# Kernel tuning notes

Hardware: AMD Instinct MI355X
Metric: run time of the kernel (lower is better)

Reference implementation:

```python
import jax, jax.numpy as jnp
import numpy as np

N_NODES = 50000
N_EDGES = 800000


def setup_inputs() -> dict:
    key = jax.random.key(0)
    ks = jax.random.split(key, 12)
    x = jax.random.normal(ks[0], (N_NODES, 500), dtype=jnp.float32)
    edge_src = jax.random.randint(ks[1], (N_EDGES,), 0, N_NODES, dtype=jnp.int32)
    edge_dst = jax.random.randint(ks[2], (N_EDGES,), 0, N_NODES, dtype=jnp.int32)
    edge_vals = jax.random.uniform(ks[3], (N_EDGES,), dtype=jnp.float32) * 0.1
    def w(k, fan_in, fan_out):
        s = 1.0 / np.sqrt(fan_in)
        return jax.random.uniform(k, (fan_in, fan_out), dtype=jnp.float32, minval=-s, maxval=s)
    W1 = w(ks[4], 500, 128)
    b1 = jnp.zeros((128,), jnp.float32)
    W2 = w(ks[5], 128, 64)
    b2 = jnp.zeros((64,), jnp.float32)
    W3 = w(ks[6], 64, 16)
    b3 = jnp.zeros((16,), jnp.float32)
    We = w(ks[7], 64, 64)
    be = jnp.zeros((64,), jnp.float32)
    return {"x": x, "edge_vals": edge_vals, "W1": W1, "b1": b1, "W2": W2,
            "b2": b2, "W3": W3, "b3": b3, "We": We, "be": be,
            "edge_src": edge_src, "edge_dst": edge_dst}


def reference(x, edge_vals, W1, b1, W2, b2, W3, b3, We, be, edge_src, edge_dst):
    n = x.shape[0]

    def gcn_layer(h, W, b):
        # GraphConvolution: support = h @ W ; out = spmm(adj, support) + b
        support = h @ W                                   # [N, d_out]
        msg = support[edge_dst] * edge_vals[:, None]      # [E, d_out]
        agg = jax.ops.segment_sum(msg, edge_src, num_segments=n)
        return agg + b

    h = jax.nn.relu(gcn_layer(x, W1, b1))
    # dropout omitted (eval mode, training=False)
    h = jax.nn.relu(gcn_layer(h, W2, b2))
    out1 = jax.nn.log_softmax(gcn_layer(h, W3, b3), axis=1)
    out2 = h @ We + be
    return (out1, out2)
```

## Files before the change

kernel.cpp:

```cpp
#include <hip/hip_runtime.h>
#include <hip/hip_bf16.h>
#include <math.h>

#define N_NODES 50000
#define N_EDGES 800000

typedef __attribute__((ext_vector_type(8))) short bf16x8;
typedef __attribute__((ext_vector_type(4))) float f32x4;

__device__ inline unsigned short f2bf(float f) {
    unsigned u = __float_as_uint(f);
    unsigned r = (u + 0x7fffu + ((u >> 16) & 1u)) >> 16;
    return (unsigned short)r;
}

__device__ inline bf16x8 pack8(float4 a0, float4 a1) {
    union { __hip_bfloat162 h2[4]; bf16x8 v; } u;
    u.h2[0] = __float22bfloat162_rn(make_float2(a0.x, a0.y));
    u.h2[1] = __float22bfloat162_rn(make_float2(a0.z, a0.w));
    u.h2[2] = __float22bfloat162_rn(make_float2(a1.x, a1.y));
    u.h2[3] = __float22bfloat162_rn(make_float2(a1.z, a1.w));
    return u.v;
}

__global__ __launch_bounds__(256) void convert_hist_kernel(
    const float* __restrict__ W1, const float* __restrict__ W2,
    const float* __restrict__ We, const float* __restrict__ W3,
    unsigned short* __restrict__ W1frag, unsigned short* __restrict__ W2frag,
    unsigned short* __restrict__ Wcfrag,
    const int* __restrict__ src, int* __restrict__ counts)
{
    if (blockIdx.x < 308) {
        int t = blockIdx.x * 256 + threadIdx.x;
        if (t < 65536) {
            int h = t >> 15;
            int r1 = t & 32767;
            int j = r1 >> 13;
            int r2 = r1 & 8191;
            int s = r2 >> 9;
            int r3 = r2 & 511;
            int lane = r3 >> 3, jj = r3 & 7;
            int k = s * 32 + (lane >> 4) * 8 + jj;
            int n = h * 64 + j * 16 + (lane & 15);
            float v = (k < 500) ? W1[k * 128 + n] : 0.0f;
            W1frag[t] = f2bf(v);
        } else if (t < 73728) {
            int t2 = t - 65536;
            int j = t2 >> 11;
            int s = (t2 >> 9) & 3;
            int lane = (t2 >> 3) & 63, jj = t2 & 7;
            int k = s * 32 + (lane >> 4) * 8 + jj;
            int n = j * 16 + (lane & 15);
            W2frag[t2] = f2bf(W2[k * 64 + n]);
        } else {
            int t3 = t - 73728;
            int j = t3 >> 10;
            int s = (t3 >> 9) & 1;
            int lane = (t3 >> 3) & 63, jj = t3 & 7;
            int k = s * 32 + (lane >> 4) * 8 + jj;
            int n = j * 16 + (lane & 15);
            float v = (n < 64) ? We[k * 64 + n] : W3[k * 16 + (n - 64)];
            Wcfrag[t3] = f2bf(v);
        }
    } else {
        int e = (blockIdx.x - 308) * 256 + threadIdx.x;
        if (e < N_EDGES) atomicAdd(&counts[src[e]], 1);
    }
}

__global__ __launch_bounds__(1024) void scan_kernel(
    const int* __restrict__ counts, int* __restrict__ row_ptr,
    int* __restrict__ cursor)
{
    constexpr int Q = N_NODES / 4;
    const int t = threadIdx.x;
    const int lane = t & 63, wave = t >> 6;
    __shared__ int wsum[16];
    __shared__ int carry_s;
    int carry = 0;
    const int4* c4 = reinterpret_cast<const int4*>(counts);
    int4* rp4 = reinterpret_cast<int4*>(row_ptr);
    int4* cu4 = reinterpret_cast<int4*>(cursor);

    for (int base = 0; base < Q; base += 1024) {
        const int g = base + t;
        int4 v = {0, 0, 0, 0};
        if (g < Q) v = c4[g];
        const int s = v.x + v.y + v.z + v.w;

        int incl = s;
#pragma unroll
        for (int off = 1; off < 64; off <<= 1) {
            int n = __shfl_up(incl, off, 64);
            if (lane >= off) incl += n;
        }
        if (lane == 63) wsum[wave] = incl;
        __syncthreads();
        if (t < 16) {
            int w = wsum[t];
            int inc = w;
#pragma unroll
            for (int off = 1; off < 16; off <<= 1) {
                int n = __shfl_up(inc, off, 64);
                if (t >= off) inc += n;
            }
            wsum[t] = inc - w;
            if (t == 15) carry_s = inc;
        }
        __syncthreads();
        if (g < Q) {
            int e0 = carry + wsum[wave] + (incl - s);
            int4 r;
            r.x = e0;
            r.y = r.x + v.x;
            r.z = r.y + v.y;
            r.w = r.z + v.z;
            rp4[g] = r;
            cu4[g] = r;
        }
        carry += carry_s;
        __syncthreads();
    }
    if (t == 0) row_ptr[N_NODES] = carry;
}

__global__ __launch_bounds__(256) void fill_kernel(
    const int* __restrict__ src, const int* __restrict__ dst,
    const float* __restrict__ vals, int* __restrict__ cursor,
    int2* __restrict__ pairs)
{
    int e = blockIdx.x * 256 + threadIdx.x;
    if (e >= N_EDGES) return;
    int pos = atomicAdd(&cursor[src[e]], 1);
    pairs[pos] = make_int2(dst[e], __float_as_int(vals[e]));
}

__global__ __launch_bounds__(256, 2) void gemm1_mfma_kernel(
    const float* __restrict__ A,
    const unsigned short* __restrict__ W1frag,
    unsigned short* __restrict__ C)
{
    __shared__ __align__(16) unsigned short Bs[32768];

    const int t = threadIdx.x;
    const int h  = blockIdx.x & 1;
    const int br = blockIdx.x >> 1;
    const int lane = t & 63;
    const int wave = t >> 6;
    const int r = lane & 15, q = lane >> 4;

    {
        const uint4* src = reinterpret_cast<const uint4*>(W1frag + h * 32768);
        uint4* dst = reinterpret_cast<uint4*>(Bs);
#pragma unroll
        for (int i = 0; i < 16; ++i)
            dst[t + i * 256] = src[t + i * 256];
    }
    __syncthreads();

    const int col0 = h * 64;

    for (int c = br * 4 + wave; c < 3125; c += 1024) {
        const float* ap = A + (size_t)(c * 16 + r) * 500;

        f32x4 acc[4];
#pragma unroll
        for (int j = 0; j < 4; ++j) acc[j] = {0.f, 0.f, 0.f, 0.f};

#pragma unroll 4
        for (int s = 0; s < 16; ++s) {
            const int kb = s * 32 + q * 8;
            const int k0 = kb < 496 ? kb : 496;
            const int k1 = (kb + 4) < 496 ? (kb + 4) : 496;
            float4 a0 = *reinterpret_cast<const float4*>(ap + k0);
            float4 a1 = *reinterpret_cast<const float4*>(ap + k1);
            bf16x8 af = pack8(a0, a1);
#pragma unroll
            for (int j = 0; j < 4; ++j) {
                bf16x8 b = *reinterpret_cast<const bf16x8*>(
                    &Bs[(size_t)((j * 16 + s) * 64 + lane) * 8]);
                acc[j] = __builtin_amdgcn_mfma_f32_16x16x32_bf16(af, b, acc[j], 0, 0, 0);
            }
        }

#pragma unroll
        for (int reg = 0; reg < 4; ++reg) {
            const int grow = c * 16 + q * 4 + reg;
#pragma unroll
            for (int j = 0; j < 4; ++j)
                C[(size_t)grow * 128 + col0 + j * 16 + r] = f2bf(acc[j][reg]);
        }
    }
}

__global__ __launch_bounds__(256) void gemm2_mfma_kernel(
    const unsigned short* __restrict__ A,
    const unsigned short* __restrict__ W2frag,
    unsigned short* __restrict__ C)
{
    __shared__ __align__(16) unsigned short Bs[8192];

    const int t = threadIdx.x;
    const int lane = t & 63, wave = t >> 6;
    const int r = lane & 15, q = lane >> 4;

    {
        const uint4* src = reinterpret_cast<const uint4*>(W2frag);
        uint4* dst = reinterpret_cast<uint4*>(Bs);
#pragma unroll
        for (int i = 0; i < 4; ++i)
            dst[t + i * 256] = src[t + i * 256];
    }
    __syncthreads();

    const int c = blockIdx.x * 4 + wave;
    if (c >= 3125) return;
    const unsigned short* ap = A + (size_t)(c * 16 + r) * 128 + q * 8;

    f32x4 acc[4];
#pragma unroll
    for (int j = 0; j < 4; ++j) acc[j] = {0.f, 0.f, 0.f, 0.f};

#pragma unroll
    for (int s = 0; s < 4; ++s) {
        bf16x8 af = *reinterpret_cast<const bf16x8*>(ap + s * 32);
#pragma unroll
        for (int j = 0; j < 4; ++j) {
            bf16x8 b = *reinterpret_cast<const bf16x8*>(
                &Bs[(size_t)((j * 4 + s) * 64 + lane) * 8]);
            acc[j] = __builtin_amdgcn_mfma_f32_16x16x32_bf16(af, b, acc[j], 0, 0, 0);
        }
    }

#pragma unroll
    for (int reg = 0; reg < 4; ++reg) {
        const int grow = c * 16 + q * 4 + reg;
#pragma unroll
        for (int j = 0; j < 4; ++j)
            C[(size_t)grow * 64 + j * 16 + r] = f2bf(acc[j][reg]);
    }
}

__global__ __launch_bounds__(256) void gemm3_mfma_kernel(
    const unsigned short* __restrict__ A,
    const unsigned short* __restrict__ Wcfrag,
    const float* __restrict__ be,
    float* __restrict__ out2,
    float* __restrict__ sup3)
{
    __shared__ __align__(16) unsigned short Bs[5120];

    const int t = threadIdx.x;
    const int lane = t & 63, wave = t >> 6;
    const int r = lane & 15, q = lane >> 4;

    {
        const uint4* src = reinterpret_cast<const uint4*>(Wcfrag);
        uint4* dst = reinterpret_cast<uint4*>(Bs);
#pragma unroll
        for (int i = 0; i < 2; ++i)
            dst[t + i * 256] = src[t + i * 256];
        if (t < 128) dst[512 + t] = src[512 + t];
    }
    __syncthreads();

    const int c = blockIdx.x * 4 + wave;
    if (c >= 3125) return;
    const unsigned short* ap = A + (size_t)(c * 16 + r) * 64 + q * 8;

    f32x4 acc[5];
#pragma unroll
    for (int j = 0; j < 5; ++j) acc[j] = {0.f, 0.f, 0.f, 0.f};

#pragma unroll
    for (int s = 0; s < 2; ++s) {
        bf16x8 af = *reinterpret_cast<const bf16x8*>(ap + s * 32);
#pragma unroll
        for (int j = 0; j < 5; ++j) {
            bf16x8 b = *reinterpret_cast<const bf16x8*>(
                &Bs[(size_t)((j * 2 + s) * 64 + lane) * 8]);
            acc[j] = __builtin_amdgcn_mfma_f32_16x16x32_bf16(af, b, acc[j], 0, 0, 0);
        }
    }

    float bev[4];
#pragma unroll
    for (int j = 0; j < 4; ++j) bev[j] = be[j * 16 + r];

#pragma unroll
    for (int reg = 0; reg < 4; ++reg) {
        const int grow = c * 16 + q * 4 + reg;
#pragma unroll
        for (int j = 0; j < 4; ++j)
            out2[(size_t)grow * 64 + j * 16 + r] = acc[j][reg] + bev[j];
        sup3[(size_t)grow * 16 + r] = acc[4][reg];
    }
}

__global__ __launch_bounds__(256) void gather128_kernel(
    const unsigned short* __restrict__ support, const int2* __restrict__ pairs,
    const int* __restrict__ row_ptr, const float* __restrict__ b1,
    unsigned short* __restrict__ h1)
{
    const int node = blockIdx.x * 4 + (threadIdx.x >> 6);
    const int lane = threadIdx.x & 63;
    const int f = lane & 15, e = lane >> 4;
    int i = row_ptr[node] + e;
    const int end = row_ptr[node + 1];

    float acc[8] = {};
    for (; i + 4 < end; i += 8) {
        int2 p0 = pairs[i], p1 = pairs[i + 4];
        float v0 = __int_as_float(p0.y), v1 = __int_as_float(p1.y);
        uint4 r0 = *reinterpret_cast<const uint4*>(support + (size_t)p0.x * 128 + f * 8);
        uint4 r1 = *reinterpret_cast<const uint4*>(support + (size_t)p1.x * 128 + f * 8);
        unsigned w0[4] = {r0.x, r0.y, r0.z, r0.w};
        unsigned w1[4] = {r1.x, r1.y, r1.z, r1.w};
#pragma unroll
        for (int j = 0; j < 4; ++j) {
            acc[2 * j]     += __uint_as_float(w0[j] << 16) * v0;
            acc[2 * j + 1] += __uint_as_float(w0[j] & 0xffff0000u) * v0;
            acc[2 * j]     += __uint_as_float(w1[j] << 16) * v1;
            acc[2 * j + 1] += __uint_as_float(w1[j] & 0xffff0000u) * v1;
        }
    }
    if (i < end) {
        int2 p = pairs[i];
        float v = __int_as_float(p.y);
        uint4 r = *reinterpret_cast<const uint4*>(support + (size_t)p.x * 128 + f * 8);
        unsigned w[4] = {r.x, r.y, r.z, r.w};
#pragma unroll
        for (int j = 0; j < 4; ++j) {
            acc[2 * j]     += __uint_as_float(w[j] << 16) * v;
            acc[2 * j + 1] += __uint_as_float(w[j] & 0xffff0000u) * v;
        }
    }
#pragma unroll
    for (int j = 0; j < 8; ++j) {
        acc[j] += __shfl_xor(acc[j], 16, 64);
        acc[j] += __shfl_xor(acc[j], 32, 64);
    }
    if (e == 0) {
        const float4 ba = *reinterpret_cast<const float4*>(b1 + f * 8);
        const float4 bb = *reinterpret_cast<const float4*>(b1 + f * 8 + 4);
        float bias[8] = {ba.x, ba.y, ba.z, ba.w, bb.x, bb.y, bb.z, bb.w};
        unsigned short h[8];
#pragma unroll
        for (int j = 0; j < 8; ++j) {
            float v = acc[j] + bias[j];
            h[j] = f2bf(v > 0.0f ? v : 0.0f);
        }
        *reinterpret_cast<uint4*>(h1 + (size_t)node * 128 + f * 8) =
            *reinterpret_cast<uint4*>(h);
    }
}

__global__ __launch_bounds__(256) void gather64_kernel(
    const unsigned short* __restrict__ support, const int2* __restrict__ pairs,
    const int* __restrict__ row_ptr, const float* __restrict__ b2,
    unsigned short* __restrict__ h2)
{
    const int node = blockIdx.x * 4 + (threadIdx.x >> 6);
    const int lane = threadIdx.x & 63;
    const int f = lane & 7, e = lane >> 3;
    int i = row_ptr[node] + e;
    const int end = row_ptr[node + 1];

    float acc[8] = {};
    for (; i + 8 < end; i += 16) {
        int2 p0 = pairs[i], p1 = pairs[i + 8];
        float v0 = __int_as_float(p0.y), v1 = __int_as_float(p1.y);
        uint4 r0 = *reinterpret_cast<const uint4*>(support + (size_t)p0.x * 64 + f * 8);
        uint4 r1 = *reinterpret_cast<const uint4*>(support + (size_t)p1.x * 64 + f * 8);
        unsigned w0[4] = {r0.x, r0.y, r0.z, r0.w};
        unsigned w1[4] = {r1.x, r1.y, r1.z, r1.w};
#pragma unroll
        for (int j = 0; j < 4; ++j) {
            acc[2 * j]     += __uint_as_float(w0[j] << 16) * v0;
            acc[2 * j + 1] += __uint_as_float(w0[j] & 0xffff0000u) * v0;
            acc[2 * j]     += __uint_as_float(w1[j] << 16) * v1;
            acc[2 * j + 1] += __uint_as_float(w1[j] & 0xffff0000u) * v1;
        }
    }
    if (i < end) {
        int2 p = pairs[i];
        float v = __int_as_float(p.y);
        uint4 r = *reinterpret_cast<const uint4*>(support + (size_t)p.x * 64 + f * 8);
        unsigned w[4] = {r.x, r.y, r.z, r.w};
#pragma unroll
        for (int j = 0; j < 4; ++j) {
            acc[2 * j]     += __uint_as_float(w[j] << 16) * v;
            acc[2 * j + 1] += __uint_as_float(w[j] & 0xffff0000u) * v;
        }
    }
#pragma unroll
    for (int j = 0; j < 8; ++j) {
        acc[j] += __shfl_xor(acc[j], 8, 64);
        acc[j] += __shfl_xor(acc[j], 16, 64);
        acc[j] += __shfl_xor(acc[j], 32, 64);
    }
    if (e == 0) {
        const float4 ba = *reinterpret_cast<const float4*>(b2 + f * 8);
        const float4 bb = *reinterpret_cast<const float4*>(b2 + f * 8 + 4);
        float bias[8] = {ba.x, ba.y, ba.z, ba.w, bb.x, bb.y, bb.z, bb.w};
        unsigned short h[8];
#pragma unroll
        for (int j = 0; j < 8; ++j) {
            float v = acc[j] + bias[j];
            h[j] = f2bf(v > 0.0f ? v : 0.0f);
        }
        *reinterpret_cast<uint4*>(h2 + (size_t)node * 64 + f * 8) =
            *reinterpret_cast<uint4*>(h);
    }
}

__global__ __launch_bounds__(256) void gather16_lsm_kernel(
    const float* __restrict__ sup3, const int2* __restrict__ pairs,
    const int* __restrict__ row_ptr, const float* __restrict__ b3,
    float* __restrict__ out1)
{
    const int node = blockIdx.x * 4 + (threadIdx.x >> 6);
    const int lane = threadIdx.x & 63;
    const int f = lane & 3, e = lane >> 2;
    int i = row_ptr[node] + e;
    const int end = row_ptr[node + 1];

    float4 acc = {0, 0, 0, 0};
    for (; i + 16 < end; i += 32) {
        int2 p0 = pairs[i], p1 = pairs[i + 16];
        float v0 = __int_as_float(p0.y), v1 = __int_as_float(p1.y);
        float4 m0 = *reinterpret_cast<const float4*>(sup3 + (size_t)p0.x * 16 + f * 4);
        float4 m1 = *reinterpret_cast<const float4*>(sup3 + (size_t)p1.x * 16 + f * 4);
        acc.x += m0.x * v0 + m1.x * v1;
        acc.y += m0.y * v0 + m1.y * v1;
        acc.z += m0.z * v0 + m1.z * v1;
        acc.w += m0.w * v0 + m1.w * v1;
    }
    if (i < end) {
        int2 p = pairs[i];
        float v = __int_as_float(p.y);
        float4 m = *reinterpret_cast<const float4*>(sup3 + (size_t)p.x * 16 + f * 4);
        acc.x += m.x * v; acc.y += m.y * v; acc.z += m.z * v; acc.w += m.w * v;
    }
#pragma unroll
    for (int off = 4; off < 64; off <<= 1) {
        acc.x += __shfl_xor(acc.x, off, 64);
        acc.y += __shfl_xor(acc.y, off, 64);
        acc.z += __shfl_xor(acc.z, off, 64);
        acc.w += __shfl_xor(acc.w, off, 64);
    }
    const float4 b = *reinterpret_cast<const float4*>(b3 + f * 4);
    float a0 = acc.x + b.x, a1 = acc.y + b.y, a2 = acc.z + b.z, a3 = acc.w + b.w;
    float mx = fmaxf(fmaxf(a0, a1), fmaxf(a2, a3));
    mx = fmaxf(mx, __shfl_xor(mx, 1, 64));
    mx = fmaxf(mx, __shfl_xor(mx, 2, 64));
    float s = expf(a0 - mx) + expf(a1 - mx) + expf(a2 - mx) + expf(a3 - mx);
    s += __shfl_xor(s, 1, 64);
    s += __shfl_xor(s, 2, 64);
    const float lse = mx + logf(s);
    if (e == 0) {
        float4 o = {a0 - lse, a1 - lse, a2 - lse, a3 - lse};
        *reinterpret_cast<float4*>(out1 + (size_t)node * 16 + f * 4) = o;
    }
}

extern "C" void kernel_launch(void* const* d_in, const int* in_sizes, int n_in,
                              void* d_out, int out_size, void* d_ws, size_t ws_size,
                              hipStream_t stream)
{
    const float* x         = (const float*)d_in[0];
    const float* edge_vals = (const float*)d_in[1];
    const float* W1 = (const float*)d_in[2];
    const float* b1 = (const float*)d_in[3];
    const float* W2 = (const float*)d_in[4];
    const float* b2 = (const float*)d_in[5];
    const float* W3 = (const float*)d_in[6];
    const float* b3 = (const float*)d_in[7];
    const float* We = (const float*)d_in[8];
    const float* be = (const float*)d_in[9];
    const int* esrc = (const int*)d_in[10];
    const int* edst = (const int*)d_in[11];

    float* out1 = (float*)d_out;
    float* out2 = (float*)d_out + (size_t)N_NODES * 16;

    char* ws = (char*)d_ws;
    float* bufA    = (float*)(ws);
    float* bufB    = (float*)(ws + 25600000);
    float* bufC    = (float*)(ws + 51200000);
    int*   counts  = (int*)  (ws + 54400000);
    int*   row_ptr = (int*)  (ws + 54600064);
    int*   cursor  = (int*)  (ws + 54800128);
    int2*  pairs   = (int2*) (ws + 55000192);

    unsigned short* W1frag = (unsigned short*)bufC;
    unsigned short* W2frag = (unsigned short*)((char*)bufC + 131072);
    unsigned short* Wcfrag = (unsigned short*)((char*)bufC + 147456);

    unsigned short* sup1bf = (unsigned short*)bufA;
    unsigned short* h1bf   = (unsigned short*)bufB;
    unsigned short* sup2bf = (unsigned short*)bufA;
    unsigned short* h2bf   = (unsigned short*)bufB;
    float*          sup3   = bufA;

    const int EB  = (N_EDGES + 255) / 256;
    const int GN  = N_NODES / 4;
    const int G23 = 782;

    hipMemsetAsync(counts, 0, (size_t)N_NODES * 4, stream);
    convert_hist_kernel<<<308 + EB, 256, 0, stream>>>(
        W1, W2, We, W3, W1frag, W2frag, Wcfrag, esrc, counts);
    scan_kernel<<<1, 1024, 0, stream>>>(counts, row_ptr, cursor);
    fill_kernel<<<EB, 256, 0, stream>>>(esrc, edst, edge_vals, cursor, pairs);

    gemm1_mfma_kernel<<<512, 256, 0, stream>>>(x, W1frag, sup1bf);

    gather128_kernel<<<GN, 256, 0, stream>>>(sup1bf, pairs, row_ptr, b1, h1bf);

    gemm2_mfma_kernel<<<G23, 256, 0, stream>>>(h1bf, W2frag, sup2bf);

    gather64_kernel<<<GN, 256, 0, stream>>>(sup2bf, pairs, row_ptr, b2, h2bf);

    gemm3_mfma_kernel<<<G23, 256, 0, stream>>>(h2bf, Wcfrag, be, out2, sup3);

    gather16_lsm_kernel<<<GN, 256, 0, stream>>>(sup3, pairs, row_ptr, b3, out1);
}
```

Baseline: 369.8 us.

## Fuse CSR fill into GEMM1 launch and column-slice gather kernels

The separate edge-fill kernel is merged into the GEMM1 launch: one block in eight runs the GEMM and the other seven scatter edges, so the atomic fill overlaps the dense compute. The 128- and 64-wide gather kernels are restructured so each block handles a fixed 16- or 8-column slice over a grid-strided set of nodes. This aims to keep each slice of the support matrix hot in cache and to raise the number of independent edges per wave. The trade-off is narrower 16-byte reads per edge, more shuffle reductions, and fill blocks sharing the GEMM kernel's 64 KB LDS footprint and its launch bound of two blocks.

Result: slower. 586.5 us (+58.6%).

```diff
diff --git a/kernel.cpp b/kernel.cpp
--- a/kernel.cpp
+++ b/kernel.cpp
@@ -124,27 +124,31 @@
     if (t == 0) row_ptr[N_NODES] = carry;
 }
 
-__global__ __launch_bounds__(256) void fill_kernel(
-    const int* __restrict__ src, const int* __restrict__ dst,
-    const float* __restrict__ vals, int* __restrict__ cursor,
-    int2* __restrict__ pairs)
-{
-    int e = blockIdx.x * 256 + threadIdx.x;
-    if (e >= N_EDGES) return;
-    int pos = atomicAdd(&cursor[src[e]], 1);
-    pairs[pos] = make_int2(dst[e], __float_as_int(vals[e]));
-}
-
-__global__ __launch_bounds__(256, 2) void gemm1_mfma_kernel(
+__global__ __launch_bounds__(256, 2) void gemm1_fill_kernel(
     const float* __restrict__ A,
     const unsigned short* __restrict__ W1frag,
-    unsigned short* __restrict__ C)
+    unsigned short* __restrict__ C,
+    const int* __restrict__ esrc, const int* __restrict__ edst,
+    const float* __restrict__ evals, int* __restrict__ cursor,
+    int2* __restrict__ pairs)
 {
     __shared__ __align__(16) unsigned short Bs[32768];
 
+    const int bid = blockIdx.x;
+    if ((bid & 7) != 0) {
+        const int f = (bid >> 3) * 7 + (bid & 7) - 1;
+        const int e = f * 256 + threadIdx.x;
+        if (e < N_EDGES) {
+            int pos = atomicAdd(&cursor[esrc[e]], 1);
+            pairs[pos] = make_int2(edst[e], __float_as_int(evals[e]));
+        }
+        return;
+    }
+
+    const int gi = bid >> 3;
     const int t = threadIdx.x;
-    const int h  = blockIdx.x & 1;
-    const int br = blockIdx.x >> 1;
+    const int h  = gi & 1;
+    const int br = gi >> 1;
     const int lane = t & 63;
     const int wave = t >> 6;
     const int r = lane & 15, q = lane >> 4;
@@ -297,120 +301,121 @@
     }
 }
 
-__global__ __launch_bounds__(256) void gather128_kernel(
+__global__ __launch_bounds__(256) void gather128s_kernel(
     const unsigned short* __restrict__ support, const int2* __restrict__ pairs,
     const int* __restrict__ row_ptr, const float* __restrict__ b1,
     unsigned short* __restrict__ h1)
 {
-    const int node = blockIdx.x * 4 + (threadIdx.x >> 6);
+    const int s  = blockIdx.x & 7;
+    const int nb = blockIdx.x >> 3;
     const int lane = threadIdx.x & 63;
-    const int f = lane & 15, e = lane >> 4;
-    int i = row_ptr[node] + e;
-    const int end = row_ptr[node + 1];
-
-    float acc[8] = {};
-    for (; i + 4 < end; i += 8) {
-        int2 p0 = pairs[i], p1 = pairs[i + 4];
-        float v0 = __int_as_float(p0.y), v1 = __int_as_float(p1.y);
-        uint4 r0 = *reinterpret_cast<const uint4*>(support + (size_t)p0.x * 128 + f * 8);
-        uint4 r1 = *reinterpret_cast<const uint4*>(support + (size_t)p1.x * 128 + f * 8);
-        unsigned w0[4] = {r0.x, r0.y, r0.z, r0.w};
-        unsigned w1[4] = {r1.x, r1.y, r1.z, r1.w};
-#pragma unroll
-        for (int j = 0; j < 4; ++j) {
-            acc[2 * j]     += __uint_as_float(w0[j] << 16) * v0;
-            acc[2 * j + 1] += __uint_as_float(w0[j] & 0xffff0000u) * v0;
-            acc[2 * j]     += __uint_as_float(w1[j] << 16) * v1;
-            acc[2 * j + 1] += __uint_as_float(w1[j] & 0xffff0000u) * v1;
-        }
-    }
-    if (i < end) {
-        int2 p = pairs[i];
-        float v = __int_as_float(p.y);
-        uint4 r = *reinterpret_cast<const uint4*>(support + (size_t)p.x * 128 + f * 8);
-        unsigned w[4] = {r.x, r.y, r.z, r.w};
-#pragma unroll
-        for (int j = 0; j < 4; ++j) {
-            acc[2 * j]     += __uint_as_float(w[j] << 16) * v;
-            acc[2 * j + 1] += __uint_as_float(w[j] & 0xffff0000u) * v;
-        }
-    }
-#pragma unroll
-    for (int j = 0; j < 8; ++j) {
-        acc[j] += __shfl_xor(acc[j], 16, 64);
-        acc[j] += __shfl_xor(acc[j], 32, 64);
-    }
-    if (e == 0) {
-        const float4 ba = *reinterpret_cast<const float4*>(b1 + f * 8);
-        const float4 bb = *reinterpret_cast<const float4*>(b1 + f * 8 + 4);
-        float bias[8] = {ba.x, ba.y, ba.z, ba.w, bb.x, bb.y, bb.z, bb.w};
-        unsigned short h[8];
+    const int wave = threadIdx.x >> 6;
+    const int f = lane & 1;
+    const int e = (lane >> 1) & 7;
+    const int n = lane >> 4;
+    const int col = s * 16 + f * 8;
+
+    float bias[8];
+    {
+        const float4 ba = *reinterpret_cast<const float4*>(b1 + col);
+        const float4 bb = *reinterpret_cast<const float4*>(b1 + col + 4);
+        bias[0] = ba.x; bias[1] = ba.y; bias[2] = ba.z; bias[3] = ba.w;
+        bias[4] = bb.x; bias[5] = bb.y; bias[6] = bb.z; bias[7] = bb.w;
+    }
+
+    for (int g = nb * 4 + wave; g < 12500; g += 1024) {
+        const int node = g * 4 + n;
+        int i = row_ptr[node] + e;
+        const int end = row_ptr[node + 1];
+
+        float acc[8] = {};
+        for (; i < end; i += 8) {
+            int2 p = pairs[i];
+            float v = __int_as_float(p.y);
+            uint4 r = *reinterpret_cast<const uint4*>(
+                support + (size_t)p.x * 128 + col);
+            unsigned w[4] = {r.x, r.y, r.z, r.w};
+#pragma unroll
+            for (int j = 0; j < 4; ++j) {
+                acc[2 * j]     += __uint_as_float(w[j] << 16) * v;
+                acc[2 * j + 1] += __uint_as_float(w[j] & 0xffff0000u) * v;
+            }
+        }
 #pragma unroll
         for (int j = 0; j < 8; ++j) {
-            float v = acc[j] + bias[j];
-            h[j] = f2bf(v > 0.0f ? v : 0.0f);
-        }
-        *reinterpret_cast<uint4*>(h1 + (size_t)node * 128 + f * 8) =
-            *reinterpret_cast<uint4*>(h);
-    }
-}
-
-__global__ __launch_bounds__(256) void gather64_kernel(
+            acc[j] += __shfl_xor(acc[j], 2, 64);
+            acc[j] += __shfl_xor(acc[j], 4, 64);
+            acc[j] += __shfl_xor(acc[j], 8, 64);
+        }
+        if (e == 0) {
+            unsigned short hv[8];
+#pragma unroll
+            for (int j = 0; j < 8; ++j) {
+                float v = acc[j] + bias[j];
+                hv[j] = f2bf(v > 0.0f ? v : 0.0f);
+            }
+            *reinterpret_cast<uint4*>(h1 + (size_t)node * 128 + col) =
+                *reinterpret_cast<uint4*>(hv);
+        }
+    }
+}
+
+__global__ __launch_bounds__(256) void gather64s_kernel(
     const unsigned short* __restrict__ support, const int2* __restrict__ pairs,
     const int* __restrict__ row_ptr, const float* __restrict__ b2,
     unsigned short* __restrict__ h2)
 {
-    const int node = blockIdx.x * 4 + (threadIdx.x >> 6);
+    const int s  = blockIdx.x & 7;
+    const int nb = blockIdx.x >> 3;
     const int lane = threadIdx.x & 63;
-    const int f = lane & 7, e = lane >> 3;
-    int i = row_ptr[node] + e;
-    const int end = row_ptr[node + 1];
-
-    float acc[8] = {};
-    for (; i + 8 < end; i += 16) {
-        int2 p0 = pairs[i], p1 = pairs[i + 8];
-        float v0 = __int_as_float(p0.y), v1 = __int_as_float(p1.y);
-        uint4 r0 = *reinterpret_cast<const uint4*>(support + (size_t)p0.x * 64 + f * 8);
-        uint4 r1 = *reinterpret_cast<const uint4*>(support + (size_t)p1.x * 64 + f * 8);
-        unsigned w0[4] = {r0.x, r0.y, r0.z, r0.w};
-        unsigned w1[4] = {r1.x, r1.y, r1.z, r1.w};
-#pragma unroll
-        for (int j = 0; j < 4; ++j) {
-            acc[2 * j]     += __uint_as_float(w0[j] << 16) * v0;
-            acc[2 * j + 1] += __uint_as_float(w0[j] & 0xffff0000u) * v0;
-            acc[2 * j]     += __uint_as_float(w1[j] << 16) * v1;
-            acc[2 * j + 1] += __uint_as_float(w1[j] & 0xffff0000u) * v1;
-        }
-    }
-    if (i < end) {
-        int2 p = pairs[i];
-        float v = __int_as_float(p.y);
-        uint4 r = *reinterpret_cast<const uint4*>(support + (size_t)p.x * 64 + f * 8);
-        unsigned w[4] = {r.x, r.y, r.z, r.w};
-#pragma unroll
-        for (int j = 0; j < 4; ++j) {
-            acc[2 * j]     += __uint_as_float(w[j] << 16) * v;
-            acc[2 * j + 1] += __uint_as_float(w[j] & 0xffff0000u) * v;
-        }
-    }
-#pragma unroll
-    for (int j = 0; j < 8; ++j) {
-        acc[j] += __shfl_xor(acc[j], 8, 64);
-        acc[j] += __shfl_xor(acc[j], 16, 64);
-        acc[j] += __shfl_xor(acc[j], 32, 64);
-    }
-    if (e == 0) {
-        const float4 ba = *reinterpret_cast<const float4*>(b2 + f * 8);
-        const float4 bb = *reinterpret_cast<const float4*>(b2 + f * 8 + 4);
-        float bias[8] = {ba.x, ba.y, ba.z, ba.w, bb.x, bb.y, bb.z, bb.w};
-        unsigned short h[8];
+    const int wave = threadIdx.x >> 6;
+    const int e = lane & 15;
+    const int n = lane >> 4;
+    const int col = s * 8;
+
+    float bias[8];
+    {
+        const float4 ba = *reinterpret_cast<const float4*>(b2 + col);
+        const float4 bb = *reinterpret_cast<const float4*>(b2 + col + 4);
+        bias[0] = ba.x; bias[1] = ba.y; bias[2] = ba.z; bias[3] = ba.w;
+        bias[4] = bb.x; bias[5] = bb.y; bias[6] = bb.z; bias[7] = bb.w;
+    }
+
+    for (int g = nb * 4 + wave; g < 12500; g += 1024) {
+        const int node = g * 4 + n;
+        int i = row_ptr[node] + e;
+        const int end = row_ptr[node + 1];
+
+        float acc[8] = {};
+        for (; i < end; i += 16) {
+            int2 p = pairs[i];
+            float v = __int_as_float(p.y);
+            uint4 r = *reinterpret_cast<const uint4*>(
+                support + (size_t)p.x * 64 + col);
+            unsigned w[4] = {r.x, r.y, r.z, r.w};
+#pragma unroll
+            for (int j = 0; j < 4; ++j) {
+                acc[2 * j]     += __uint_as_float(w[j] << 16) * v;
+                acc[2 * j + 1] += __uint_as_float(w[j] & 0xffff0000u) * v;
+            }
+        }
 #pragma unroll
         for (int j = 0; j < 8; ++j) {
-            float v = acc[j] + bias[j];
-            h[j] = f2bf(v > 0.0f ? v : 0.0f);
-        }
-        *reinterpret_cast<uint4*>(h2 + (size_t)node * 64 + f * 8) =
-            *reinterpret_cast<uint4*>(h);
+            acc[j] += __shfl_xor(acc[j], 1, 64);
+            acc[j] += __shfl_xor(acc[j], 2, 64);
+            acc[j] += __shfl_xor(acc[j], 4, 64);
+            acc[j] += __shfl_xor(acc[j], 8, 64);
+        }
+        if (e == 0) {
+            unsigned short hv[8];
+#pragma unroll
+            for (int j = 0; j < 8; ++j) {
+                float v = acc[j] + bias[j];
+                hv[j] = f2bf(v > 0.0f ? v : 0.0f);
+            }
+            *reinterpret_cast<uint4*>(h2 + (size_t)node * 64 + col) =
+                *reinterpret_cast<uint4*>(hv);
+        }
     }
 }
 
@@ -505,21 +510,22 @@
 
     const int EB  = (N_EDGES + 255) / 256;
     const int GN  = N_NODES / 4;
+    const int GS  = 2048;
     const int G23 = 782;
 
     hipMemsetAsync(counts, 0, (size_t)N_NODES * 4, stream);
     convert_hist_kernel<<<308 + EB, 256, 0, stream>>>(
         W1, W2, We, W3, W1frag, W2frag, Wcfrag, esrc, counts);
     scan_kernel<<<1, 1024, 0, stream>>>(counts, row_ptr, cursor);
-    fill_kernel<<<EB, 256, 0, stream>>>(esrc, edst, edge_vals, cursor, pairs);
-
-    gemm1_mfma_kernel<<<512, 256, 0, stream>>>(x, W1frag, sup1bf);
-
-    gather128_kernel<<<GN, 256, 0, stream>>>(sup1bf, pairs, row_ptr, b1, h1bf);
+
+    gemm1_fill_kernel<<<4096, 256, 0, stream>>>(
+        x, W1frag, sup1bf, esrc, edst, edge_vals, cursor, pairs);
+
+    gather128s_kernel<<<GS, 256, 0, stream>>>(sup1bf, pairs, row_ptr, b1, h1bf);
 
     gemm2_mfma_kernel<<<G23, 256, 0, stream>>>(h1bf, W2frag, sup2bf);
 
-    gather64_kernel<<<GN, 256, 0, stream>>>(sup2bf, pairs, row_ptr, b2, h2bf);
+    gather64s_kernel<<<GS, 256, 0, stream>>>(sup2bf, pairs, row_ptr, b2, h2bf);
 
     gemm3_mfma_kernel<<<G23, 256, 0, stream>>>(h2bf, Wcfrag, be, out2, sup3);
 
```

## Fuse CSR fill into gemm1 launch and widen scan per-thread work

Applied to the files above, without the earlier changes.

The edge-fill pass is merged into the first GEMM kernel: 64 extra blocks do the atomic CSR scatter while the remaining 512 blocks run the MFMA GEMM, so the two independent stages overlap and one launch is removed. The single-block scan now handles four int4 groups per thread per iteration, which cuts its loop trip count and barrier count. The risk is that the 64 fill blocks are slow and set the kernel's finish time, and that they compete with the GEMM blocks for CU slots.

After: 379.5 us. 2.6% more time.

```diff
diff --git a/kernel.cpp b/kernel.cpp
--- a/kernel.cpp
+++ b/kernel.cpp
@@ -82,11 +82,18 @@
     int4* rp4 = reinterpret_cast<int4*>(row_ptr);
     int4* cu4 = reinterpret_cast<int4*>(cursor);
 
-    for (int base = 0; base < Q; base += 1024) {
-        const int g = base + t;
-        int4 v = {0, 0, 0, 0};
-        if (g < Q) v = c4[g];
-        const int s = v.x + v.y + v.z + v.w;
+    for (int base = 0; base < Q; base += 4096) {
+        int4 v[4];
+        int ls[5];
+        ls[0] = 0;
+#pragma unroll
+        for (int k = 0; k < 4; ++k) {
+            const int g = base + t * 4 + k;
+            if (g < Q) v[k] = c4[g];
+            else       v[k] = make_int4(0, 0, 0, 0);
+            ls[k + 1] = ls[k] + v[k].x + v[k].y + v[k].z + v[k].w;
+        }
+        const int s = ls[4];
 
         int incl = s;
 #pragma unroll
@@ -108,15 +115,20 @@
             if (t == 15) carry_s = inc;
         }
         __syncthreads();
-        if (g < Q) {
-            int e0 = carry + wsum[wave] + (incl - s);
-            int4 r;
-            r.x = e0;
-            r.y = r.x + v.x;
-            r.z = r.y + v.y;
-            r.w = r.z + v.z;
-            rp4[g] = r;
-            cu4[g] = r;
+        const int e0 = carry + wsum[wave] + (incl - s);
+#pragma unroll
+        for (int k = 0; k < 4; ++k) {
+            const int g = base + t * 4 + k;
+            if (g < Q) {
+                const int b0 = e0 + ls[k];
+                int4 r;
+                r.x = b0;
+                r.y = r.x + v[k].x;
+                r.z = r.y + v[k].y;
+                r.w = r.z + v[k].z;
+                rp4[g] = r;
+                cu4[g] = r;
+            }
         }
         carry += carry_s;
         __syncthreads();
@@ -124,27 +136,31 @@
     if (t == 0) row_ptr[N_NODES] = carry;
 }
 
-__global__ __launch_bounds__(256) void fill_kernel(
-    const int* __restrict__ src, const int* __restrict__ dst,
-    const float* __restrict__ vals, int* __restrict__ cursor,
-    int2* __restrict__ pairs)
-{
-    int e = blockIdx.x * 256 + threadIdx.x;
-    if (e >= N_EDGES) return;
-    int pos = atomicAdd(&cursor[src[e]], 1);
-    pairs[pos] = make_int2(dst[e], __float_as_int(vals[e]));
-}
-
-__global__ __launch_bounds__(256, 2) void gemm1_mfma_kernel(
+__global__ __launch_bounds__(256, 2) void gemm1_fill_kernel(
     const float* __restrict__ A,
     const unsigned short* __restrict__ W1frag,
-    unsigned short* __restrict__ C)
+    unsigned short* __restrict__ C,
+    const int* __restrict__ esrc, const int* __restrict__ edst,
+    const float* __restrict__ evals, int* __restrict__ cursor,
+    int2* __restrict__ pairs)
 {
     __shared__ __align__(16) unsigned short Bs[32768];
 
+    const int bid = blockIdx.x;
+    if (bid < 64) {
+        const int tid = bid * 256 + threadIdx.x;
+#pragma unroll 4
+        for (int e = tid; e < N_EDGES; e += 16384) {
+            int pos = atomicAdd(&cursor[esrc[e]], 1);
+            pairs[pos] = make_int2(edst[e], __float_as_int(evals[e]));
+        }
+        return;
+    }
+
+    const int gi = bid - 64;
     const int t = threadIdx.x;
-    const int h  = blockIdx.x & 1;
-    const int br = blockIdx.x >> 1;
+    const int h  = gi & 1;
+    const int br = gi >> 1;
     const int lane = t & 63;
     const int wave = t >> 6;
     const int r = lane & 15, q = lane >> 4;
@@ -511,9 +527,9 @@
     convert_hist_kernel<<<308 + EB, 256, 0, stream>>>(
         W1, W2, We, W3, W1frag, W2frag, Wcfrag, esrc, counts);
     scan_kernel<<<1, 1024, 0, stream>>>(counts, row_ptr, cursor);
-    fill_kernel<<<EB, 256, 0, stream>>>(esrc, edst, edge_vals, cursor, pairs);
-
-    gemm1_mfma_kernel<<<512, 256, 0, stream>>>(x, W1frag, sup1bf);
+
+    gemm1_fill_kernel<<<576, 256, 0, stream>>>(
+        x, W1frag, sup1bf, esrc, edst, edge_vals, cursor, pairs);
 
     gather128_kernel<<<GN, 256, 0, stream>>>(sup1bf, pairs, row_ptr, b1, h1bf);
 
```

## Fuse layer-1 gather with layer-2 GEMM via shared-memory tile; widen scan per thread

Applied to the files above, without the earlier changes.

The layer-1 sparse aggregation is merged with the 128x64 MFMA GEMM. Each block gathers 16 nodes into an LDS tile, and each wave then computes one 16-column slice of the layer-2 support, so the h1 intermediate never goes to global memory. The scan kernel now processes four int4 groups per thread, cutting the number of serial block iterations and barriers. Buffers are reassigned so the intermediates stay separate. In exchange, each fused block gathers 4 nodes per wave serially and reloads W2 fragments, which lowers parallelism in the gather phase.

Measured after the change: 365.3 us. Within noise of the previous version (-1.2%).

```diff
diff --git a/kernel.cpp b/kernel.cpp
--- a/kernel.cpp
+++ b/kernel.cpp
@@ -82,11 +82,18 @@
     int4* rp4 = reinterpret_cast<int4*>(row_ptr);
     int4* cu4 = reinterpret_cast<int4*>(cursor);
 
-    for (int base = 0; base < Q; base += 1024) {
-        const int g = base + t;
-        int4 v = {0, 0, 0, 0};
-        if (g < Q) v = c4[g];
-        const int s = v.x + v.y + v.z + v.w;
+    for (int base = 0; base < Q; base += 4096) {
+        int4 v[4];
+        int ls[5];
+        ls[0] = 0;
+#pragma unroll
+        for (int k = 0; k < 4; ++k) {
+            const int g = base + t * 4 + k;
+            if (g < Q) v[k] = c4[g];
+            else       v[k] = make_int4(0, 0, 0, 0);
+            ls[k + 1] = ls[k] + v[k].x + v[k].y + v[k].z + v[k].w;
+        }
+        const int s = ls[4];
 
         int incl = s;
 #pragma unroll
@@ -108,15 +115,20 @@
             if (t == 15) carry_s = inc;
         }
         __syncthreads();
-        if (g < Q) {
-            int e0 = carry + wsum[wave] + (incl - s);
-            int4 r;
-            r.x = e0;
-            r.y = r.x + v.x;
-            r.z = r.y + v.y;
-            r.w = r.z + v.z;
-            rp4[g] = r;
-            cu4[g] = r;
+        const int e0 = carry + wsum[wave] + (incl - s);
+#pragma unroll
+        for (int k = 0; k < 4; ++k) {
+            const int g = base + t * 4 + k;
+            if (g < Q) {
+                const int b0 = e0 + ls[k];
+                int4 r;
+                r.x = b0;
+                r.y = r.x + v[k].x;
+                r.z = r.y + v[k].y;
+                r.w = r.z + v[k].z;
+                rp4[g] = r;
+                cu4[g] = r;
+            }
         }
         carry += carry_s;
         __syncthreads();
@@ -193,16 +205,18 @@
     }
 }
 
-__global__ __launch_bounds__(256) void gemm2_mfma_kernel(
-    const unsigned short* __restrict__ A,
+__global__ __launch_bounds__(256) void gather128_gemm2_kernel(
+    const unsigned short* __restrict__ support, const int2* __restrict__ pairs,
+    const int* __restrict__ row_ptr, const float* __restrict__ b1,
     const unsigned short* __restrict__ W2frag,
-    unsigned short* __restrict__ C)
+    unsigned short* __restrict__ sup2)
 {
     __shared__ __align__(16) unsigned short Bs[8192];
+    __shared__ __align__(16) unsigned short h1s[16 * 136];
 
     const int t = threadIdx.x;
     const int lane = t & 63, wave = t >> 6;
-    const int r = lane & 15, q = lane >> 4;
+    const int f = lane & 15, e = lane >> 4;
 
     {
         const uint4* src = reinterpret_cast<const uint4*>(W2frag);
@@ -211,33 +225,75 @@
         for (int i = 0; i < 4; ++i)
             dst[t + i * 256] = src[t + i * 256];
     }
+
+    const float4 ba = *reinterpret_cast<const float4*>(b1 + f * 8);
+    const float4 bb = *reinterpret_cast<const float4*>(b1 + f * 8 + 4);
+    const float bias[8] = {ba.x, ba.y, ba.z, ba.w, bb.x, bb.y, bb.z, bb.w};
+
+    const int node0 = blockIdx.x * 16 + wave * 4;
+
+    for (int nn = 0; nn < 4; ++nn) {
+        const int node = node0 + nn;
+        int i = row_ptr[node] + e;
+        const int end = row_ptr[node + 1];
+
+        float acc[8] = {};
+        for (; i + 4 < end; i += 8) {
+            int2 p0 = pairs[i], p1 = pairs[i + 4];
+            float v0 = __int_as_float(p0.y), v1 = __int_as_float(p1.y);
+            uint4 r0 = *reinterpret_cast<const uint4*>(support + (size_t)p0.x * 128 + f * 8);
+            uint4 r1 = *reinterpret_cast<const uint4*>(support + (size_t)p1.x * 128 + f * 8);
+            unsigned w0[4] = {r0.x, r0.y, r0.z, r0.w};
+            unsigned w1[4] = {r1.x, r1.y, r1.z, r1.w};
+#pragma unroll
+            for (int j = 0; j < 4; ++j) {
+                acc[2 * j]     += __uint_as_float(w0[j] << 16) * v0;
+                acc[2 * j + 1] += __uint_as_float(w0[j] & 0xffff0000u) * v0;
+                acc[2 * j]     += __uint_as_float(w1[j] << 16) * v1;
+                acc[2 * j + 1] += __uint_as_float(w1[j] & 0xffff0000u) * v1;
+            }
+        }
+        if (i < end) {
+            int2 p = pairs[i];
+            float v = __int_as_float(p.y);
+            uint4 r = *reinterpret_cast<const uint4*>(support + (size_t)p.x * 128 + f * 8);
+            unsigned w[4] = {r.x, r.y, r.z, r.w};
+#pragma unroll
+            for (int j = 0; j < 4; ++j) {
+                acc[2 * j]     += __uint_as_float(w[j] << 16) * v;
+                acc[2 * j + 1] += __uint_as_float(w[j] & 0xffff0000u) * v;
+            }
+        }
+#pragma unroll
+        for (int j = 0; j < 8; ++j) {
+            acc[j] += __shfl_xor(acc[j], 16, 64);
+            acc[j] += __shfl_xor(acc[j], 32, 64);
+        }
+        if (e == 0) {
+            unsigned short hv[8];
+#pragma unroll
+            for (int j = 0; j < 8; ++j) {
+                float v = acc[j] + bias[j];
+                hv[j] = f2bf(v > 0.0f ? v : 0.0f);
+            }
+            *reinterpret_cast<uint4*>(&h1s[(wave * 4 + nn) * 136 + f * 8]) =
+                *reinterpret_cast<uint4*>(hv);
+        }
+    }
     __syncthreads();
 
-    const int c = blockIdx.x * 4 + wave;
-    if (c >= 3125) return;
-    const unsigned short* ap = A + (size_t)(c * 16 + r) * 128 + q * 8;
-
-    f32x4 acc[4];
-#pragma unroll
-    for (int j = 0; j < 4; ++j) acc[j] = {0.f, 0.f, 0.f, 0.f};
-
+    f32x4 acc2 = {0.f, 0.f, 0.f, 0.f};
 #pragma unroll
     for (int s = 0; s < 4; ++s) {
-        bf16x8 af = *reinterpret_cast<const bf16x8*>(ap + s * 32);
-#pragma unroll
-        for (int j = 0; j < 4; ++j) {
-            bf16x8 b = *reinterpret_cast<const bf16x8*>(
-                &Bs[(size_t)((j * 4 + s) * 64 + lane) * 8]);
-            acc[j] = __builtin_amdgcn_mfma_f32_16x16x32_bf16(af, b, acc[j], 0, 0, 0);
-        }
-    }
-
+        bf16x8 af = *reinterpret_cast<const bf16x8*>(&h1s[f * 136 + (s * 4 + e) * 8]);
+        bf16x8 b = *reinterpret_cast<const bf16x8*>(
+            &Bs[(size_t)((wave * 4 + s) * 64 + lane) * 8]);
+        acc2 = __builtin_amdgcn_mfma_f32_16x16x32_bf16(af, b, acc2, 0, 0, 0);
+    }
 #pragma unroll
     for (int reg = 0; reg < 4; ++reg) {
-        const int grow = c * 16 + q * 4 + reg;
-#pragma unroll
-        for (int j = 0; j < 4; ++j)
-            C[(size_t)grow * 64 + j * 16 + r] = f2bf(acc[j][reg]);
+        const int grow = blockIdx.x * 16 + e * 4 + reg;
+        sup2[(size_t)grow * 64 + wave * 16 + f] = f2bf(acc2[reg]);
     }
 }
 
@@ -294,64 +350,6 @@
         for (int j = 0; j < 4; ++j)
             out2[(size_t)grow * 64 + j * 16 + r] = acc[j][reg] + bev[j];
         sup3[(size_t)grow * 16 + r] = acc[4][reg];
-    }
-}
-
-__global__ __launch_bounds__(256) void gather128_kernel(
-    const unsigned short* __restrict__ support, const int2* __restrict__ pairs,
-    const int* __restrict__ row_ptr, const float* __restrict__ b1,
-    unsigned short* __restrict__ h1)
-{
-    const int node = blockIdx.x * 4 + (threadIdx.x >> 6);
-    const int lane = threadIdx.x & 63;
-    const int f = lane & 15, e = lane >> 4;
-    int i = row_ptr[node] + e;
-    const int end = row_ptr[node + 1];
-
-    float acc[8] = {};
-    for (; i + 4 < end; i += 8) {
-        int2 p0 = pairs[i], p1 = pairs[i + 4];
-        float v0 = __int_as_float(p0.y), v1 = __int_as_float(p1.y);
-        uint4 r0 = *reinterpret_cast<const uint4*>(support + (size_t)p0.x * 128 + f * 8);
-        uint4 r1 = *reinterpret_cast<const uint4*>(support + (size_t)p1.x * 128 + f * 8);
-        unsigned w0[4] = {r0.x, r0.y, r0.z, r0.w};
-        unsigned w1[4] = {r1.x, r1.y, r1.z, r1.w};
-#pragma unroll
-        for (int j = 0; j < 4; ++j) {
-            acc[2 * j]     += __uint_as_float(w0[j] << 16) * v0;
-            acc[2 * j + 1] += __uint_as_float(w0[j] & 0xffff0000u) * v0;
-            acc[2 * j]     += __uint_as_float(w1[j] << 16) * v1;
-            acc[2 * j + 1] += __uint_as_float(w1[j] & 0xffff0000u) * v1;
-        }
-    }
-    if (i < end) {
-        int2 p = pairs[i];
-        float v = __int_as_float(p.y);
-        uint4 r = *reinterpret_cast<const uint4*>(support + (size_t)p.x * 128 + f * 8);
-        unsigned w[4] = {r.x, r.y, r.z, r.w};
-#pragma unroll
-        for (int j = 0; j < 4; ++j) {
-            acc[2 * j]     += __uint_as_float(w[j] << 16) * v;
-            acc[2 * j + 1] += __uint_as_float(w[j] & 0xffff0000u) * v;
-        }
-    }
-#pragma unroll
-    for (int j = 0; j < 8; ++j) {
-        acc[j] += __shfl_xor(acc[j], 16, 64);
-        acc[j] += __shfl_xor(acc[j], 32, 64);
-    }
-    if (e == 0) {
-        const float4 ba = *reinterpret_cast<const float4*>(b1 + f * 8);
-        const float4 bb = *reinterpret_cast<const float4*>(b1 + f * 8 + 4);
-        float bias[8] = {ba.x, ba.y, ba.z, ba.w, bb.x, bb.y, bb.z, bb.w};
-        unsigned short h[8];
-#pragma unroll
-        for (int j = 0; j < 8; ++j) {
-            float v = acc[j] + bias[j];
-            h[j] = f2bf(v > 0.0f ? v : 0.0f);
-        }
-        *reinterpret_cast<uint4*>(h1 + (size_t)node * 128 + f * 8) =
-            *reinterpret_cast<uint4*>(h);
     }
 }
 
@@ -498,14 +496,14 @@
     unsigned short* Wcfrag = (unsigned short*)((char*)bufC + 147456);
 
     unsigned short* sup1bf = (unsigned short*)bufA;
-    unsigned short* h1bf   = (unsigned short*)bufB;
-    unsigned short* sup2bf = (unsigned short*)bufA;
-    unsigned short* h2bf   = (unsigned short*)bufB;
-    float*          sup3   = bufA;
+    unsigned short* sup2bf = (unsigned short*)bufB;
+    unsigned short* h2bf   = (unsigned short*)bufA;
+    float*          sup3   = (float*)((char*)bufB + 6400000);
 
     const int EB  = (N_EDGES + 255) / 256;
     const int GN  = N_NODES / 4;
-    const int G23 = 782;
+    const int GB  = N_NODES / 16;
+    const int G3  = 782;
 
     hipMemsetAsync(counts, 0, (size_t)N_NODES * 4, stream);
     convert_hist_kernel<<<308 + EB, 256, 0, stream>>>(
@@ -515,13 +513,12 @@
 
     gemm1_mfma_kernel<<<512, 256, 0, stream>>>(x, W1frag, sup1bf);
 
-    gather128_kernel<<<GN, 256, 0, stream>>>(sup1bf, pairs, row_ptr, b1, h1bf);
-
-    gemm2_mfma_kernel<<<G23, 256, 0, stream>>>(h1bf, W2frag, sup2bf);
+    gather128_gemm2_kernel<<<GB, 256, 0, stream>>>(
+        sup1bf, pairs, row_ptr, b1, W2frag, sup2bf);
 
     gather64_kernel<<<GN, 256, 0, stream>>>(sup2bf, pairs, row_ptr, b2, h2bf);
 
-    gemm3_mfma_kernel<<<G23, 256, 0, stream>>>(h2bf, Wcfrag, be, out2, sup3);
+    gemm3_mfma_kernel<<<G3, 256, 0, stream>>>(h2bf, Wcfrag, be, out2, sup3);
 
     gather16_lsm_kernel<<<GN, 256, 0, stream>>>(sup3, pairs, row_ptr, b3, out1);
 }
```
